# Kernel tuning notes

Measured on AMD Instinct MI355X. Metric: run time of the kernel, lower is better.

The kernel has to match this reference:

```python
import jax, jax.numpy as jnp
import numpy as np

B, T, K = 128, 512, 256  # batch, seq_len, num_tags


def setup_inputs() -> dict:
    key = jax.random.key(0)
    k1, k2, k3 = jax.random.split(key, 3)
    y_pred = jax.random.normal(k1, (B, T, K), dtype=jnp.float32)
    trans = jax.random.normal(k2, (K, K), dtype=jnp.float32)
    y_true = jax.random.randint(k3, (B, T), 0, K)
    return {"y_pred": y_pred, "trans": trans, "y_true": y_true}


def reference(y_pred, trans, y_true):
    # sparse_loss: one-hot the integer labels
    num_tags = trans.shape[0]
    y_oh = jax.nn.one_hot(y_true, num_tags, dtype=y_pred.dtype)  # [B,T,K]

    # dense_loss: mask frames where all logits <= -1e6
    mask = jnp.all(y_pred > -1e6, axis=2, keepdims=True).astype(y_pred.dtype)  # [B,T,1]
    y_oh = y_oh * mask
    yp = y_pred * mask

    # target_score: emission score + transition score along the gold path
    point_score = jnp.einsum('bti,bti->b', y_oh, yp)
    trans_score = jnp.einsum('bti,ij,btj->b', y_oh[:, :-1], trans, y_oh[:, 1:])
    target_score = point_score + trans_score  # [B]

    # log_norm_step: forward algorithm (log-semiring recurrence) via scan
    init = yp[:, 0]  # [B,K]

    def step(alpha, xm):
        x, m = xm  # x: [B,K] emissions at t, m: [B,1] mask at t
        # logsumexp over previous tag: alpha[b,i] + trans[i,j]
        new = jax.nn.logsumexp(alpha[:, :, None] + trans[None, :, :], axis=1) + x
        alpha = m * new + (1.0 - m) * alpha
        return alpha, None

    xs = (jnp.swapaxes(yp[:, 1:], 0, 1), jnp.swapaxes(mask[:, 1:], 0, 1))  # time-major
    last_alpha, _ = jax.lax.scan(step, init, xs)  # [B,K]
    log_norm = jax.nn.logsumexp(last_alpha, axis=1)  # [B]

    return log_norm - target_score  # per-example CRF negative log-likelihood [B]
```

## Files before the change

kernel.cpp:

```cpp
#include <hip/hip_runtime.h>
#include <stdint.h>

#define T_ 512
#define K_ 256
#define NB 16
#define WROW 264
#define L2E 1.4426950408889634f
#define LN2 0.6931471805599453f

typedef __attribute__((ext_vector_type(8))) short short8;
typedef __attribute__((ext_vector_type(4))) float f32x4;

__device__ __forceinline__ float fexp2(float x) {
#if __has_builtin(__builtin_amdgcn_exp2f)
  return __builtin_amdgcn_exp2f(x);
#else
  return exp2f(x);
#endif
}
__device__ __forceinline__ float flog2(float x) {
#if __has_builtin(__builtin_amdgcn_logf)
  return __builtin_amdgcn_logf(x);
#else
  return log2f(x);
#endif
}
__device__ __forceinline__ unsigned int umax_(unsigned int a, unsigned int b) {
  return a > b ? a : b;
}
__device__ __forceinline__ unsigned short f2bf(float f) {
  union { float f; uint32_t u; } v; v.f = f;
  uint32_t r = v.u + 0x7fffu + ((v.u >> 16) & 1u);
  return (unsigned short)(r >> 16);
}
__device__ __forceinline__ uint32_t cvt_pk_bf16(float a, float b) {
  uint32_t d;
  asm("v_cvt_pk_bf16_f32 %0, %1, %2" : "=v"(d) : "v"(a), "v"(b));
  return d;
}

#define BAR() do { \
  asm volatile("s_waitcnt lgkmcnt(0)" ::: "memory"); \
  __builtin_amdgcn_s_barrier(); \
  asm volatile("" ::: "memory"); \
} while (0)


__global__ void prep_E(const float* __restrict__ trans, unsigned short* __restrict__ Efrag) {
  int idx = blockIdx.x * 256 + threadIdx.x;
  int e = idx & 7;
  int ln = (idx >> 3) & 63;
  int kb = (idx >> 9) & 7;
  int mt = idx >> 12;
  int j = mt * 16 + (ln & 15);
  int k = kb * 32 + ((ln >> 4) << 3) + e;
  Efrag[idx] = f2bf(__expf(trans[k * K_ + j]));
}

__global__ void aux_mask(const float* __restrict__ yp, unsigned char* __restrict__ masks) {
  int item = blockIdx.x * 4 + (threadIdx.x >> 6);
  int lane = threadIdx.x & 63;
  const float4 v = *(const float4*)(yp + (size_t)item * K_ + lane * 4);
  float mn = fminf(fminf(v.x, v.y), fminf(v.z, v.w));
  unsigned long long bl = __ballot(mn > -1000000.0f);
  if (lane == 0) {
    int b = item >> 9, t = item & 511;
    masks[t * 128 + b] = (bl == ~0ull) ? 1 : 0;
  }
}

__global__ void aux_score(const float* __restrict__ yp, const float* __restrict__ trans,
                          const int* __restrict__ ytrue, const unsigned char* __restrict__ masks,
                          float* __restrict__ score) {
  int b = blockIdx.x;
  int lane = threadIdx.x;
  float s = 0.f;
  #pragma unroll
  for (int k = 0; k < 8; ++k) {
    int t = lane + 64 * k;
    int y = ytrue[b * T_ + t];
    int m = masks[t * 128 + b];
    float x = yp[((size_t)b * T_ + t) * K_ + y];
    if (m) s += x;
    if (t >= 1) {
      int ym = ytrue[b * T_ + t - 1];
      int mm = masks[(t - 1) * 128 + b];
      if (m && mm) s += trans[ym * K_ + y];
    }
  }
  #pragma unroll
  for (int off = 32; off; off >>= 1) s += __shfl_xor(s, off, 64);
  if (lane == 0) score[b] = s;
}


template<int TM4, bool RESC, bool MWR, bool MASKED>
__device__ __forceinline__ void crf_step(
    int t, int c, int g, int wv, const int* tb,
    const short8 (&Ef)[2][8],
    float (&a)[8], float (&exf)[8], int& acc, int& mkc,
    const float* xb, float4 (&XN)[2], float4 (&XI)[2],
    unsigned short (*Wl)[NB * WROW], const unsigned char* mkl, unsigned int* Mpart) {
  BAR();
  if (RESC) {
    unsigned int Mx = Mpart[c];
    #pragma unroll
    for (int w = 1; w < 8; ++w) Mx = umax_(Mx, Mpart[w * NB + c]);
    unsigned int e_ = Mx >> 23;
    float sf = __builtin_bit_cast(float, (254u - e_) << 23);
    if (!MASKED || mkc) acc += 127 - (int)e_;
    #pragma unroll
    for (int j = 0; j < 8; ++j) exf[j] *= sf;
  }
  f32x4 ac0 = {0.f, 0.f, 0.f, 0.f}, ac1 = {0.f, 0.f, 0.f, 0.f};
  {
    const unsigned short* rrow = &Wl[TM4 & 1][c * WROW];
    #pragma unroll
    for (int kb = 0; kb < 8; ++kb) {
      short8 bf = __builtin_bit_cast(short8, *(const uint4*)(&rrow[kb * 32 + g * 8]));
      ac0 = __builtin_amdgcn_mfma_f32_16x16x32_bf16(Ef[0][kb], bf, ac0, 0, 0, 0);
      ac1 = __builtin_amdgcn_mfma_f32_16x16x32_bf16(Ef[1][kb], bf, ac1, 0, 0, 0);
    }
  }
  if (MASKED) {
    #pragma unroll
    for (int i = 0; i < 4; ++i) { float an = ac0[i] * exf[i];     a[i]     = mkc ? an : a[i]; }
    #pragma unroll
    for (int i = 0; i < 4; ++i) { float an = ac1[i] * exf[4 + i]; a[4 + i] = mkc ? an : a[4 + i]; }
  } else {
    #pragma unroll
    for (int i = 0; i < 4; ++i) a[i]     = ac0[i] * exf[i];
    #pragma unroll
    for (int i = 0; i < 4; ++i) a[4 + i] = ac1[i] * exf[4 + i];
  }
  {
    unsigned short* wrow = &Wl[(TM4 + 1) & 1][c * WROW];
    #pragma unroll
    for (int m = 0; m < 2; ++m) {
      uint2 pp;
      pp.x = cvt_pk_bf16(a[4 * m + 0], a[4 * m + 1]);
      pp.y = cvt_pk_bf16(a[4 * m + 2], a[4 * m + 3]);
      *(uint2*)(&wrow[tb[m]]) = pp;
    }
  }
  if (MWR) {
    unsigned int pm = __builtin_bit_cast(uint32_t, a[0]);
    #pragma unroll
    for (int j = 1; j < 8; ++j) pm = umax_(pm, __builtin_bit_cast(uint32_t, a[j]));
    pm = umax_(pm, (unsigned int)__shfl_xor((int)pm, 16, 64));
    pm = umax_(pm, (unsigned int)__shfl_xor((int)pm, 32, 64));
    if (g == 0) Mpart[wv * NB + c] = pm;
  }
  #pragma unroll
  for (int m = 0; m < 2; ++m) {
    exf[4 * m + 0] = fexp2(XN[m].x * L2E);
    exf[4 * m + 1] = fexp2(XN[m].y * L2E);
    exf[4 * m + 2] = fexp2(XN[m].z * L2E);
    exf[4 * m + 3] = fexp2(XN[m].w * L2E);
  }
  if (MASKED) mkc = mkl[(t + 1 < T_ ? t + 1 : 0) * NB + c];
  {
    int tt = t + 4;
    tt = tt > (T_ - 1) ? (T_ - 1) : tt;
    #pragma unroll
    for (int m = 0; m < 2; ++m)
      XI[m] = *(const float4*)(xb + (size_t)tt * K_ + tb[m]);
  }
}

template<bool MASKED>
__device__ __forceinline__ void scan_run(
    int tid, int c, int g, int wv, const int* tb, int b0,
    const short8 (&Ef)[2][8], const float* xb,
    float4 (&xinit)[2], float4 (&X0q)[2], float4 (&X1q)[2],
    float4 (&X2q)[2], float4 (&X3q)[2],
    unsigned short (*Wl)[NB * WROW], const unsigned char* mkl,
    unsigned int* Mpart, float* Spart,
    const float* __restrict__ score, float* __restrict__ out) {
  float a[8], exf[8];
  int acc = 0;
  int mkc = 0;
  {
    int mk0 = MASKED ? mkl[c] : 1;
    #pragma unroll
    for (int m = 0; m < 2; ++m) {
      float e0 = fexp2(xinit[m].x * L2E);
      float e1 = fexp2(xinit[m].y * L2E);
      float e2 = fexp2(xinit[m].z * L2E);
      float e3 = fexp2(xinit[m].w * L2E);
      a[4 * m + 0] = (MASKED && !mk0) ? 1.0f : e0;
      a[4 * m + 1] = (MASKED && !mk0) ? 1.0f : e1;
      a[4 * m + 2] = (MASKED && !mk0) ? 1.0f : e2;
      a[4 * m + 3] = (MASKED && !mk0) ? 1.0f : e3;
    }
  }
  {
    unsigned short* wrow = &Wl[1][c * WROW];
    #pragma unroll
    for (int m = 0; m < 2; ++m) {
      uint2 pp;
      pp.x = cvt_pk_bf16(a[4 * m + 0], a[4 * m + 1]);
      pp.y = cvt_pk_bf16(a[4 * m + 2], a[4 * m + 3]);
      *(uint2*)(&wrow[tb[m]]) = pp;
    }
  }
  #pragma unroll
  for (int m = 0; m < 2; ++m) {
    exf[4 * m + 0] = fexp2(X1q[m].x * L2E);
    exf[4 * m + 1] = fexp2(X1q[m].y * L2E);
    exf[4 * m + 2] = fexp2(X1q[m].z * L2E);
    exf[4 * m + 3] = fexp2(X1q[m].w * L2E);
  }
  if (MASKED) mkc = mkl[NB + c];

  crf_step<1, false, false, MASKED>(1, c, g, wv, tb, Ef, a, exf, acc, mkc, xb, X2q, X1q, Wl, mkl, Mpart);
  crf_step<2, false, false, MASKED>(2, c, g, wv, tb, Ef, a, exf, acc, mkc, xb, X3q, X2q, Wl, mkl, Mpart);
  crf_step<3, false, true , MASKED>(3, c, g, wv, tb, Ef, a, exf, acc, mkc, xb, X0q, X3q, Wl, mkl, Mpart);

  #pragma unroll 1
  for (int t0 = 4; t0 < T_; t0 += 4) {
    crf_step<0, true , false, MASKED>(t0,     c, g, wv, tb, Ef, a, exf, acc, mkc, xb, X1q, X0q, Wl, mkl, Mpart);
    crf_step<1, false, false, MASKED>(t0 + 1, c, g, wv, tb, Ef, a, exf, acc, mkc, xb, X2q, X1q, Wl, mkl, Mpart);
    crf_step<2, false, false, MASKED>(t0 + 2, c, g, wv, tb, Ef, a, exf, acc, mkc, xb, X3q, X2q, Wl, mkl, Mpart);
    crf_step<3, false, true , MASKED>(t0 + 3, c, g, wv, tb, Ef, a, exf, acc, mkc, xb, X0q, X3q, Wl, mkl, Mpart);
  }

  __syncthreads();
  {
    float ssum = 0.f;
    #pragma unroll
    for (int j = 0; j < 8; ++j) ssum += a[j];
    ssum += __shfl_xor(ssum, 16, 64);
    ssum += __shfl_xor(ssum, 32, 64);
    if (g == 0) Spart[wv * NB + c] = ssum;
  }
  __syncthreads();
  if (tid < NB) {
    float S = 0.f;
    #pragma unroll
    for (int w = 0; w < 8; ++w) S += Spart[w * NB + tid];
    out[b0 + tid] = LN2 * (flog2(S) - (float)acc) - score[b0 + tid];
  }
}

__global__ __launch_bounds__(512, 1) void crf_scan(
    const float* __restrict__ yp, const unsigned short* __restrict__ Efrag,
    const unsigned char* __restrict__ masks, const float* __restrict__ score,
    float* __restrict__ out) {
  const int b0 = blockIdx.x * NB;
  const int tid = threadIdx.x;
  const int wv = tid >> 6, lane = tid & 63;
  const int c = lane & 15;
  const int g = lane >> 4;

  __shared__ unsigned short Wl[2][NB * WROW];
  __shared__ unsigned char mkl[T_ * NB];
  __shared__ unsigned int Mpart[8 * NB];
  __shared__ float Spart[8 * NB];
  __shared__ int sflag[8];

  short8 Ef[2][8];
  {
    const uint4* ep = (const uint4*)Efrag;
    #pragma unroll
    for (int m = 0; m < 2; ++m)
      #pragma unroll
      for (int kb = 0; kb < 8; ++kb)
        Ef[m][kb] = __builtin_bit_cast(short8, ep[((wv * 2 + m) * 8 + kb) * 64 + lane]);
  }

  uint4 md0;
  {
    uint4* dst = (uint4*)mkl;
    md0 = *(const uint4*)(masks + tid * 128 + b0);
    dst[tid] = md0;
  }

  const float* xb = yp + (size_t)(b0 + c) * T_ * K_;
  int tb[2];
  #pragma unroll
  for (int m = 0; m < 2; ++m) tb[m] = wv * 32 + m * 16 + g * 4;

  float4 xinit[2], X0q[2], X1q[2], X2q[2], X3q[2];
  #pragma unroll
  for (int m = 0; m < 2; ++m) xinit[m] = *(const float4*)(xb + tb[m]);
  #pragma unroll
  for (int m = 0; m < 2; ++m) X1q[m] = *(const float4*)(xb + 1 * K_ + tb[m]);
  #pragma unroll
  for (int m = 0; m < 2; ++m) X2q[m] = *(const float4*)(xb + 2 * K_ + tb[m]);
  #pragma unroll
  for (int m = 0; m < 2; ++m) X3q[m] = *(const float4*)(xb + 3 * K_ + tb[m]);
  #pragma unroll
  for (int m = 0; m < 2; ++m) X0q[m] = *(const float4*)(xb + 4 * K_ + tb[m]);

  {
    uint32_t w = md0.x & md0.y & md0.z & md0.w;
    unsigned long long bl = __ballot(w == 0x01010101u);
    if (lane == 0) sflag[wv] = (bl == ~0ull) ? 1 : 0;
  }
  __syncthreads();
  bool allm = true;
  #pragma unroll
  for (int w = 0; w < 8; ++w) allm = allm && sflag[w];

  if (allm) {
    scan_run<false>(tid, c, g, wv, tb, b0, Ef, xb, xinit, X0q, X1q, X2q, X3q,
                    Wl, mkl, Mpart, Spart, score, out);
  } else {
    scan_run<true>(tid, c, g, wv, tb, b0, Ef, xb, xinit, X0q, X1q, X2q, X3q,
                   Wl, mkl, Mpart, Spart, score, out);
  }
}

extern "C" void kernel_launch(void* const* d_in, const int* in_sizes, int n_in,
                              void* d_out, int out_size, void* d_ws, size_t ws_size,
                              hipStream_t stream) {
  const float* yp = (const float*)d_in[0];
  const float* trans = (const float*)d_in[1];
  const int* ytrue = (const int*)d_in[2];
  float* out = (float*)d_out;

  unsigned short* Efrag = (unsigned short*)d_ws;
  unsigned char* masks = (unsigned char*)d_ws + 131072;
  float* score = (float*)((char*)d_ws + 131072 + 65536);

  prep_E<<<dim3(256), dim3(256), 0, stream>>>(trans, Efrag);
  aux_mask<<<dim3(16384), dim3(256), 0, stream>>>(yp, masks);
  aux_score<<<dim3(128), dim3(64), 0, stream>>>(yp, trans, ytrue, masks, score);
  crf_scan<<<dim3(8), dim3(512), 0, stream>>>(yp, Efrag, masks, score, out);
}
```

Measured before the change: 302.0 us.

## Switch CRF scan recurrence to FP8 MFMA with per-step rescaling and precomputed exp emissions

Stores exp(trans) as e4m3 and the alpha vector as bf8 in LDS, so the recurrence uses the fp8×bf8 16x16x32 MFMA instead of bf16, halving the LDS and register traffic per step. Because bf8 has little dynamic range, rescaling by the running max now happens every step, using double-buffered partial maxima, instead of every fourth step. Emission exponentials are optionally precomputed as bf16 inside the mask kernel, which runs at full occupancy, when workspace allows, so the serial scan does less transcendental work and loads half the bytes. The cost is much lower numerical precision, which risks tolerance failures, plus an extra 32 MB workspace write and read.

```diff
diff --git a/kernel.cpp b/kernel.cpp
--- a/kernel.cpp
+++ b/kernel.cpp
@@ -4,11 +4,10 @@
 #define T_ 512
 #define K_ 256
 #define NB 16
-#define WROW 264
+#define WSTRIDE 272
 #define L2E 1.4426950408889634f
 #define LN2 0.6931471805599453f
 
-typedef __attribute__((ext_vector_type(8))) short short8;
 typedef __attribute__((ext_vector_type(4))) float f32x4;
 
 __device__ __forceinline__ float fexp2(float x) {
@@ -28,15 +27,48 @@
 __device__ __forceinline__ unsigned int umax_(unsigned int a, unsigned int b) {
   return a > b ? a : b;
 }
-__device__ __forceinline__ unsigned short f2bf(float f) {
-  union { float f; uint32_t u; } v; v.f = f;
-  uint32_t r = v.u + 0x7fffu + ((v.u >> 16) & 1u);
-  return (unsigned short)(r >> 16);
-}
+__device__ __forceinline__ float bits2f(uint32_t u) { return __builtin_bit_cast(float, u); }
+__device__ __forceinline__ uint32_t f2bits(float f) { return __builtin_bit_cast(uint32_t, f); }
+
 __device__ __forceinline__ uint32_t cvt_pk_bf16(float a, float b) {
   uint32_t d;
   asm("v_cvt_pk_bf16_f32 %0, %1, %2" : "=v"(d) : "v"(a), "v"(b));
   return d;
+}
+
+template<bool HI>
+__device__ __forceinline__ uint32_t pk_bf8(float a, float b, uint32_t old) {
+#if __has_builtin(__builtin_amdgcn_cvt_pk_bf8_f32)
+  return (uint32_t)__builtin_amdgcn_cvt_pk_bf8_f32(a, b, (int)old, HI);
+#else
+  unsigned short ha = __builtin_bit_cast(unsigned short, (_Float16)fminf(a, 57344.0f));
+  unsigned short hb = __builtin_bit_cast(unsigned short, (_Float16)fminf(b, 57344.0f));
+  uint32_t ra = (((uint32_t)ha + 0x7Fu + ((ha >> 8) & 1u)) >> 8) & 0xFFu;
+  uint32_t rb = (((uint32_t)hb + 0x7Fu + ((hb >> 8) & 1u)) >> 8) & 0xFFu;
+  uint32_t v = ra | (rb << 8);
+  return HI ? ((old & 0x0000FFFFu) | (v << 16)) : ((old & 0xFFFF0000u) | v);
+#endif
+}
+
+__device__ unsigned char to_e4m3(float f) {
+  if (!(f > 0.0f)) return 0;
+  if (f >= 448.0f) return 0x7E;
+  uint32_t u = f2bits(f);
+  int e = (int)((u >> 23) & 255) - 127;
+  uint32_t m = u & 0x7fffff;
+  if (e < -6) {
+    int s2 = 20 + (-6 - e);
+    if (s2 >= 24) return 0;
+    uint32_t full = 0x800000u | m;
+    uint32_t q = full >> s2, r = full & ((1u << s2) - 1);
+    uint32_t half = 1u << (s2 - 1);
+    q += (r > half || (r == half && (q & 1))) ? 1u : 0u;
+    return (unsigned char)q;
+  }
+  uint32_t q = m >> 20, r = m & 0xFFFFFu;
+  q += (r > 0x80000u || (r == 0x80000u && (q & 1))) ? 1u : 0u;
+  if (q == 8) { q = 0; e += 1; if (e > 8) return 0x7E; }
+  return (unsigned char)(((e + 7) << 3) | q);
 }
 
 #define BAR() do { \
@@ -46,7 +78,7 @@
 } while (0)
 
 
-__global__ void prep_E(const float* __restrict__ trans, unsigned short* __restrict__ Efrag) {
+__global__ void prep_E(const float* __restrict__ trans, unsigned char* __restrict__ Efrag) {
   int idx = blockIdx.x * 256 + threadIdx.x;
   int e = idx & 7;
   int ln = (idx >> 3) & 63;
@@ -54,10 +86,11 @@
   int mt = idx >> 12;
   int j = mt * 16 + (ln & 15);
   int k = kb * 32 + ((ln >> 4) << 3) + e;
-  Efrag[idx] = f2bf(__expf(trans[k * K_ + j]));
-}
-
-__global__ void aux_mask(const float* __restrict__ yp, unsigned char* __restrict__ masks) {
+  Efrag[idx] = to_e4m3(__expf(trans[k * K_ + j]));
+}
+
+__global__ void aux_mask_exf(const float* __restrict__ yp, unsigned char* __restrict__ masks,
+                             unsigned short* __restrict__ exf, int write_exf) {
   int item = blockIdx.x * 4 + (threadIdx.x >> 6);
   int lane = threadIdx.x & 63;
   const float4 v = *(const float4*)(yp + (size_t)item * K_ + lane * 4);
@@ -66,6 +99,12 @@
   if (lane == 0) {
     int b = item >> 9, t = item & 511;
     masks[t * 128 + b] = (bl == ~0ull) ? 1 : 0;
+  }
+  if (write_exf) {
+    uint2 p;
+    p.x = cvt_pk_bf16(fexp2(v.x * L2E), fexp2(v.y * L2E));
+    p.y = cvt_pk_bf16(fexp2(v.z * L2E), fexp2(v.w * L2E));
+    *(uint2*)(exf + (size_t)item * K_ + lane * 4) = p;
   }
 }
 
@@ -94,135 +133,168 @@
 }
 
 
-template<int TM4, bool RESC, bool MWR, bool MASKED>
+template<bool PRE> struct Slot;
+template<> struct Slot<true>  { uint2 u0, u1; };
+template<> struct Slot<false> { float4 f0, f1; };
+
+template<bool PRE>
+__device__ __forceinline__ void slot_load(Slot<PRE>& s, const void* base, int tt, int off0) {
+  if constexpr (PRE) {
+    const unsigned short* p = (const unsigned short*)base + (size_t)tt * K_ + off0;
+    s.u0 = *(const uint2*)(p);
+    s.u1 = *(const uint2*)(p + 16);
+  } else {
+    const float* p = (const float*)base + (size_t)tt * K_ + off0;
+    s.f0 = *(const float4*)(p);
+    s.f1 = *(const float4*)(p + 16);
+  }
+}
+
+template<bool PRE>
+__device__ __forceinline__ void slot_exf(const Slot<PRE>& s, float (&exf)[8]) {
+  if constexpr (PRE) {
+    exf[0] = bits2f(s.u0.x << 16); exf[1] = bits2f(s.u0.x & 0xffff0000u);
+    exf[2] = bits2f(s.u0.y << 16); exf[3] = bits2f(s.u0.y & 0xffff0000u);
+    exf[4] = bits2f(s.u1.x << 16); exf[5] = bits2f(s.u1.x & 0xffff0000u);
+    exf[6] = bits2f(s.u1.y << 16); exf[7] = bits2f(s.u1.y & 0xffff0000u);
+  } else {
+    exf[0] = fexp2(s.f0.x * L2E); exf[1] = fexp2(s.f0.y * L2E);
+    exf[2] = fexp2(s.f0.z * L2E); exf[3] = fexp2(s.f0.w * L2E);
+    exf[4] = fexp2(s.f1.x * L2E); exf[5] = fexp2(s.f1.y * L2E);
+    exf[6] = fexp2(s.f1.z * L2E); exf[7] = fexp2(s.f1.w * L2E);
+  }
+}
+
+__device__ __forceinline__ void pack_w(const float (&a)[8], unsigned char* wrow, int wv, int g) {
+  float s0 = fminf(a[0], 57344.f), s1 = fminf(a[1], 57344.f);
+  float s2 = fminf(a[2], 57344.f), s3 = fminf(a[3], 57344.f);
+  float s4 = fminf(a[4], 57344.f), s5 = fminf(a[5], 57344.f);
+  float s6 = fminf(a[6], 57344.f), s7 = fminf(a[7], 57344.f);
+  uint32_t u0 = pk_bf8<false>(s0, s1, 0u); u0 = pk_bf8<true>(s2, s3, u0);
+  uint32_t u1 = pk_bf8<false>(s4, s5, 0u); u1 = pk_bf8<true>(s6, s7, u1);
+  *(uint32_t*)(wrow + 32 * wv + 4 * g) = u0;
+  *(uint32_t*)(wrow + 32 * wv + 16 + 4 * g) = u1;
+}
+
+template<int TM4, bool MASKED, bool PRE>
 __device__ __forceinline__ void crf_step(
-    int t, int c, int g, int wv, const int* tb,
-    const short8 (&Ef)[2][8],
+    int t, int c, int g, int wv, int off0,
+    const uint2 (&Ef)[2][8],
     float (&a)[8], float (&exf)[8], int& acc, int& mkc,
-    const float* xb, float4 (&XN)[2], float4 (&XI)[2],
-    unsigned short (*Wl)[NB * WROW], const unsigned char* mkl, unsigned int* Mpart) {
+    const void* xbase, Slot<PRE>& XN, Slot<PRE>& XI,
+    unsigned char (*Wl)[NB * WSTRIDE], const unsigned char* mkl,
+    unsigned int (*Mpart)[NB][8]) {
   BAR();
-  if (RESC) {
-    unsigned int Mx = Mpart[c];
-    #pragma unroll
-    for (int w = 1; w < 8; ++w) Mx = umax_(Mx, Mpart[w * NB + c]);
-    unsigned int e_ = Mx >> 23;
-    float sf = __builtin_bit_cast(float, (254u - e_) << 23);
-    if (!MASKED || mkc) acc += 127 - (int)e_;
-    #pragma unroll
-    for (int j = 0; j < 8; ++j) exf[j] *= sf;
-  }
+  unsigned int Mx;
+  {
+    const uint4* mp = (const uint4*)&Mpart[(TM4 + 1) & 1][c][0];
+    uint4 m0 = mp[0], m1 = mp[1];
+    Mx = umax_(umax_(umax_(m0.x, m0.y), umax_(m0.z, m0.w)),
+               umax_(umax_(m1.x, m1.y), umax_(m1.z, m1.w)));
+  }
+  unsigned int e_ = Mx >> 23;
+  float sfp = bits2f((248u - e_) << 23);
+  int scur = 121 - (int)e_;
   f32x4 ac0 = {0.f, 0.f, 0.f, 0.f}, ac1 = {0.f, 0.f, 0.f, 0.f};
   {
-    const unsigned short* rrow = &Wl[TM4 & 1][c * WROW];
+    const unsigned char* rrow = &Wl[TM4 & 1][c * WSTRIDE];
     #pragma unroll
     for (int kb = 0; kb < 8; ++kb) {
-      short8 bf = __builtin_bit_cast(short8, *(const uint4*)(&rrow[kb * 32 + g * 8]));
-      ac0 = __builtin_amdgcn_mfma_f32_16x16x32_bf16(Ef[0][kb], bf, ac0, 0, 0, 0);
-      ac1 = __builtin_amdgcn_mfma_f32_16x16x32_bf16(Ef[1][kb], bf, ac1, 0, 0, 0);
+      long bf = *(const long*)(rrow + kb * 32 + g * 8);
+      ac0 = __builtin_amdgcn_mfma_f32_16x16x32_fp8_bf8(
+          __builtin_bit_cast(long, Ef[0][kb]), bf, ac0, 0, 0, 0);
+      ac1 = __builtin_amdgcn_mfma_f32_16x16x32_fp8_bf8(
+          __builtin_bit_cast(long, Ef[1][kb]), bf, ac1, 0, 0, 0);
     }
   }
   if (MASKED) {
     #pragma unroll
-    for (int i = 0; i < 4; ++i) { float an = ac0[i] * exf[i];     a[i]     = mkc ? an : a[i]; }
-    #pragma unroll
-    for (int i = 0; i < 4; ++i) { float an = ac1[i] * exf[4 + i]; a[4 + i] = mkc ? an : a[4 + i]; }
+    for (int i = 0; i < 4; ++i) { float an = ac0[i] * exf[i] * sfp;     a[i]     = mkc ? an : a[i]; }
+    #pragma unroll
+    for (int i = 0; i < 4; ++i) { float an = ac1[i] * exf[4 + i] * sfp; a[4 + i] = mkc ? an : a[4 + i]; }
+    if (mkc) acc += scur;
   } else {
     #pragma unroll
-    for (int i = 0; i < 4; ++i) a[i]     = ac0[i] * exf[i];
-    #pragma unroll
-    for (int i = 0; i < 4; ++i) a[4 + i] = ac1[i] * exf[4 + i];
-  }
-  {
-    unsigned short* wrow = &Wl[(TM4 + 1) & 1][c * WROW];
-    #pragma unroll
-    for (int m = 0; m < 2; ++m) {
-      uint2 pp;
-      pp.x = cvt_pk_bf16(a[4 * m + 0], a[4 * m + 1]);
-      pp.y = cvt_pk_bf16(a[4 * m + 2], a[4 * m + 3]);
-      *(uint2*)(&wrow[tb[m]]) = pp;
-    }
-  }
-  if (MWR) {
-    unsigned int pm = __builtin_bit_cast(uint32_t, a[0]);
-    #pragma unroll
-    for (int j = 1; j < 8; ++j) pm = umax_(pm, __builtin_bit_cast(uint32_t, a[j]));
+    for (int i = 0; i < 4; ++i) a[i]     = ac0[i] * exf[i] * sfp;
+    #pragma unroll
+    for (int i = 0; i < 4; ++i) a[4 + i] = ac1[i] * exf[4 + i] * sfp;
+    acc += scur;
+  }
+  pack_w(a, &Wl[(TM4 + 1) & 1][c * WSTRIDE], wv, g);
+  {
+    unsigned int pm = f2bits(a[0]);
+    #pragma unroll
+    for (int j = 1; j < 8; ++j) pm = umax_(pm, f2bits(a[j]));
     pm = umax_(pm, (unsigned int)__shfl_xor((int)pm, 16, 64));
     pm = umax_(pm, (unsigned int)__shfl_xor((int)pm, 32, 64));
-    if (g == 0) Mpart[wv * NB + c] = pm;
-  }
-  #pragma unroll
-  for (int m = 0; m < 2; ++m) {
-    exf[4 * m + 0] = fexp2(XN[m].x * L2E);
-    exf[4 * m + 1] = fexp2(XN[m].y * L2E);
-    exf[4 * m + 2] = fexp2(XN[m].z * L2E);
-    exf[4 * m + 3] = fexp2(XN[m].w * L2E);
-  }
+    if (g == 0) Mpart[TM4 & 1][c][wv] = pm;
+  }
+  slot_exf<PRE>(XN, exf);
   if (MASKED) mkc = mkl[(t + 1 < T_ ? t + 1 : 0) * NB + c];
   {
     int tt = t + 4;
     tt = tt > (T_ - 1) ? (T_ - 1) : tt;
-    #pragma unroll
-    for (int m = 0; m < 2; ++m)
-      XI[m] = *(const float4*)(xb + (size_t)tt * K_ + tb[m]);
-  }
-}
-
-template<bool MASKED>
+    slot_load<PRE>(XI, xbase, tt, off0);
+  }
+}
+
+template<bool MASKED, bool PRE>
 __device__ __forceinline__ void scan_run(
-    int tid, int c, int g, int wv, const int* tb, int b0,
-    const short8 (&Ef)[2][8], const float* xb,
-    float4 (&xinit)[2], float4 (&X0q)[2], float4 (&X1q)[2],
-    float4 (&X2q)[2], float4 (&X3q)[2],
-    unsigned short (*Wl)[NB * WROW], const unsigned char* mkl,
-    unsigned int* Mpart, float* Spart,
+    int tid, int c, int g, int wv, int off0, int b0,
+    const uint2 (&Ef)[2][8], const void* xbase,
+    Slot<PRE>& Sinit, Slot<PRE>& S0, Slot<PRE>& S1, Slot<PRE>& S2, Slot<PRE>& S3,
+    unsigned char (*Wl)[NB * WSTRIDE], const unsigned char* mkl,
+    unsigned int (*Mpart)[NB][8], float* Spart,
     const float* __restrict__ score, float* __restrict__ out) {
   float a[8], exf[8];
-  int acc = 0;
-  int mkc = 0;
-  {
+  int acc = 0, mkc = 0;
+  {
+    float e0[8];
+    slot_exf<PRE>(Sinit, e0);
     int mk0 = MASKED ? mkl[c] : 1;
     #pragma unroll
-    for (int m = 0; m < 2; ++m) {
-      float e0 = fexp2(xinit[m].x * L2E);
-      float e1 = fexp2(xinit[m].y * L2E);
-      float e2 = fexp2(xinit[m].z * L2E);
-      float e3 = fexp2(xinit[m].w * L2E);
-      a[4 * m + 0] = (MASKED && !mk0) ? 1.0f : e0;
-      a[4 * m + 1] = (MASKED && !mk0) ? 1.0f : e1;
-      a[4 * m + 2] = (MASKED && !mk0) ? 1.0f : e2;
-      a[4 * m + 3] = (MASKED && !mk0) ? 1.0f : e3;
-    }
-  }
-  {
-    unsigned short* wrow = &Wl[1][c * WROW];
-    #pragma unroll
-    for (int m = 0; m < 2; ++m) {
-      uint2 pp;
-      pp.x = cvt_pk_bf16(a[4 * m + 0], a[4 * m + 1]);
-      pp.y = cvt_pk_bf16(a[4 * m + 2], a[4 * m + 3]);
-      *(uint2*)(&wrow[tb[m]]) = pp;
-    }
-  }
+    for (int j = 0; j < 8; ++j) a[j] = (MASKED && !mk0) ? 1.0f : e0[j];
+  }
+  unsigned int pm0;
+  {
+    unsigned int pm = f2bits(a[0]);
+    #pragma unroll
+    for (int j = 1; j < 8; ++j) pm = umax_(pm, f2bits(a[j]));
+    pm = umax_(pm, (unsigned int)__shfl_xor((int)pm, 16, 64));
+    pm = umax_(pm, (unsigned int)__shfl_xor((int)pm, 32, 64));
+    pm0 = pm;
+    if (g == 0) Mpart[0][c][wv] = pm;
+  }
+  __syncthreads();
+  float sfp0;
+  {
+    unsigned int Mx;
+    const uint4* mp = (const uint4*)&Mpart[0][c][0];
+    uint4 m0 = mp[0], m1 = mp[1];
+    Mx = umax_(umax_(umax_(m0.x, m0.y), umax_(m0.z, m0.w)),
+               umax_(umax_(m1.x, m1.y), umax_(m1.z, m1.w)));
+    unsigned int e_ = Mx >> 23;
+    sfp0 = bits2f((248u - e_) << 23);
+    acc = 121 - (int)e_;
+  }
+  __syncthreads();
   #pragma unroll
-  for (int m = 0; m < 2; ++m) {
-    exf[4 * m + 0] = fexp2(X1q[m].x * L2E);
-    exf[4 * m + 1] = fexp2(X1q[m].y * L2E);
-    exf[4 * m + 2] = fexp2(X1q[m].z * L2E);
-    exf[4 * m + 3] = fexp2(X1q[m].w * L2E);
-  }
+  for (int j = 0; j < 8; ++j) a[j] *= sfp0;
+  if (g == 0) Mpart[0][c][wv] = f2bits(bits2f(pm0) * sfp0);
+  pack_w(a, &Wl[1][c * WSTRIDE], wv, g);
+  slot_exf<PRE>(S1, exf);
   if (MASKED) mkc = mkl[NB + c];
 
-  crf_step<1, false, false, MASKED>(1, c, g, wv, tb, Ef, a, exf, acc, mkc, xb, X2q, X1q, Wl, mkl, Mpart);
-  crf_step<2, false, false, MASKED>(2, c, g, wv, tb, Ef, a, exf, acc, mkc, xb, X3q, X2q, Wl, mkl, Mpart);
-  crf_step<3, false, true , MASKED>(3, c, g, wv, tb, Ef, a, exf, acc, mkc, xb, X0q, X3q, Wl, mkl, Mpart);
+  crf_step<1, MASKED, PRE>(1, c, g, wv, off0, Ef, a, exf, acc, mkc, xbase, S2, S1, Wl, mkl, Mpart);
+  crf_step<2, MASKED, PRE>(2, c, g, wv, off0, Ef, a, exf, acc, mkc, xbase, S3, S2, Wl, mkl, Mpart);
+  crf_step<3, MASKED, PRE>(3, c, g, wv, off0, Ef, a, exf, acc, mkc, xbase, S0, S3, Wl, mkl, Mpart);
 
   #pragma unroll 1
   for (int t0 = 4; t0 < T_; t0 += 4) {
-    crf_step<0, true , false, MASKED>(t0,     c, g, wv, tb, Ef, a, exf, acc, mkc, xb, X1q, X0q, Wl, mkl, Mpart);
-    crf_step<1, false, false, MASKED>(t0 + 1, c, g, wv, tb, Ef, a, exf, acc, mkc, xb, X2q, X1q, Wl, mkl, Mpart);
-    crf_step<2, false, false, MASKED>(t0 + 2, c, g, wv, tb, Ef, a, exf, acc, mkc, xb, X3q, X2q, Wl, mkl, Mpart);
-    crf_step<3, false, true , MASKED>(t0 + 3, c, g, wv, tb, Ef, a, exf, acc, mkc, xb, X0q, X3q, Wl, mkl, Mpart);
+    crf_step<0, MASKED, PRE>(t0,     c, g, wv, off0, Ef, a, exf, acc, mkc, xbase, S1, S0, Wl, mkl, Mpart);
+    crf_step<1, MASKED, PRE>(t0 + 1, c, g, wv, off0, Ef, a, exf, acc, mkc, xbase, S2, S1, Wl, mkl, Mpart);
+    crf_step<2, MASKED, PRE>(t0 + 2, c, g, wv, off0, Ef, a, exf, acc, mkc, xbase, S3, S2, Wl, mkl, Mpart);
+    crf_step<3, MASKED, PRE>(t0 + 3, c, g, wv, off0, Ef, a, exf, acc, mkc, xbase, S0, S3, Wl, mkl, Mpart);
   }
 
   __syncthreads();
@@ -243,30 +315,32 @@
   }
 }
 
+template<bool PRE>
 __global__ __launch_bounds__(512, 1) void crf_scan(
-    const float* __restrict__ yp, const unsigned short* __restrict__ Efrag,
-    const unsigned char* __restrict__ masks, const float* __restrict__ score,
-    float* __restrict__ out) {
+    const float* __restrict__ yp, const unsigned char* __restrict__ Efrag,
+    const unsigned char* __restrict__ masks, const unsigned short* __restrict__ exfp,
+    const float* __restrict__ score, float* __restrict__ out) {
   const int b0 = blockIdx.x * NB;
   const int tid = threadIdx.x;
   const int wv = tid >> 6, lane = tid & 63;
   const int c = lane & 15;
   const int g = lane >> 4;
-
-  __shared__ unsigned short Wl[2][NB * WROW];
+  const int off0 = 32 * wv + 4 * g;
+
+  __shared__ unsigned char Wl[2][NB * WSTRIDE];
   __shared__ unsigned char mkl[T_ * NB];
-  __shared__ unsigned int Mpart[8 * NB];
+  __shared__ unsigned int Mpart[2][NB][8];
   __shared__ float Spart[8 * NB];
   __shared__ int sflag[8];
 
-  short8 Ef[2][8];
-  {
-    const uint4* ep = (const uint4*)Efrag;
+  uint2 Ef[2][8];
+  {
+    const uint2* ep = (const uint2*)Efrag;
     #pragma unroll
     for (int m = 0; m < 2; ++m)
       #pragma unroll
       for (int kb = 0; kb < 8; ++kb)
-        Ef[m][kb] = __builtin_bit_cast(short8, ep[((wv * 2 + m) * 8 + kb) * 64 + lane]);
+        Ef[m][kb] = ep[((wv * 2 + m) * 8 + kb) * 64 + lane];
   }
 
   uint4 md0;
@@ -276,22 +350,16 @@
     dst[tid] = md0;
   }
 
-  const float* xb = yp + (size_t)(b0 + c) * T_ * K_;
-  int tb[2];
-  #pragma unroll
-  for (int m = 0; m < 2; ++m) tb[m] = wv * 32 + m * 16 + g * 4;
-
-  float4 xinit[2], X0q[2], X1q[2], X2q[2], X3q[2];
-  #pragma unroll
-  for (int m = 0; m < 2; ++m) xinit[m] = *(const float4*)(xb + tb[m]);
-  #pragma unroll
-  for (int m = 0; m < 2; ++m) X1q[m] = *(const float4*)(xb + 1 * K_ + tb[m]);
-  #pragma unroll
-  for (int m = 0; m < 2; ++m) X2q[m] = *(const float4*)(xb + 2 * K_ + tb[m]);
-  #pragma unroll
-  for (int m = 0; m < 2; ++m) X3q[m] = *(const float4*)(xb + 3 * K_ + tb[m]);
-  #pragma unroll
-  for (int m = 0; m < 2; ++m) X0q[m] = *(const float4*)(xb + 4 * K_ + tb[m]);
+  const void* xbase;
+  if constexpr (PRE) xbase = (const void*)(exfp + (size_t)(b0 + c) * T_ * K_);
+  else               xbase = (const void*)(yp + (size_t)(b0 + c) * T_ * K_);
+
+  Slot<PRE> Sinit, S0, S1, S2, S3;
+  slot_load<PRE>(Sinit, xbase, 0, off0);
+  slot_load<PRE>(S1, xbase, 1, off0);
+  slot_load<PRE>(S2, xbase, 2, off0);
+  slot_load<PRE>(S3, xbase, 3, off0);
+  slot_load<PRE>(S0, xbase, 4, off0);
 
   {
     uint32_t w = md0.x & md0.y & md0.z & md0.w;
@@ -304,11 +372,11 @@
   for (int w = 0; w < 8; ++w) allm = allm && sflag[w];
 
   if (allm) {
-    scan_run<false>(tid, c, g, wv, tb, b0, Ef, xb, xinit, X0q, X1q, X2q, X3q,
-                    Wl, mkl, Mpart, Spart, score, out);
+    scan_run<false, PRE>(tid, c, g, wv, off0, b0, Ef, xbase, Sinit, S0, S1, S2, S3,
+                         Wl, mkl, Mpart, Spart, score, out);
   } else {
-    scan_run<true>(tid, c, g, wv, tb, b0, Ef, xb, xinit, X0q, X1q, X2q, X3q,
-                   Wl, mkl, Mpart, Spart, score, out);
+    scan_run<true, PRE>(tid, c, g, wv, off0, b0, Ef, xbase, Sinit, S0, S1, S2, S3,
+                        Wl, mkl, Mpart, Spart, score, out);
   }
 }
 
@@ -320,12 +388,20 @@
   const int* ytrue = (const int*)d_in[2];
   float* out = (float*)d_out;
 
-  unsigned short* Efrag = (unsigned short*)d_ws;
-  unsigned char* masks = (unsigned char*)d_ws + 131072;
-  float* score = (float*)((char*)d_ws + 131072 + 65536);
+  unsigned char* Efrag = (unsigned char*)d_ws;
+  unsigned char* masks = (unsigned char*)d_ws + 65536;
+  float* score = (float*)((char*)d_ws + 131072);
+  unsigned short* exf = (unsigned short*)((char*)d_ws + 131584);
+
+  const size_t exf_bytes = (size_t)128 * T_ * K_ * sizeof(unsigned short);
+  const bool pre = ws_size >= 131584 + exf_bytes;
 
   prep_E<<<dim3(256), dim3(256), 0, stream>>>(trans, Efrag);
-  aux_mask<<<dim3(16384), dim3(256), 0, stream>>>(yp, masks);
+  aux_mask_exf<<<dim3(16384), dim3(256), 0, stream>>>(yp, masks, exf, pre ? 1 : 0);
   aux_score<<<dim3(128), dim3(64), 0, stream>>>(yp, trans, ytrue, masks, score);
-  crf_scan<<<dim3(8), dim3(512), 0, stream>>>(yp, Efrag, masks, score, out);
-}
+  if (pre) {
+    crf_scan<true><<<dim3(8), dim3(512), 0, stream>>>(yp, Efrag, masks, exf, score, out);
+  } else {
+    crf_scan<false><<<dim3(8), dim3(512), 0, stream>>>(yp, Efrag, masks, exf, score, out);
+  }
+}
```

Result: slower. 321.0 us (+6.3%).

## Interleave two independent 16-sequence scans per block to hide step latency

Applied to the files above, without the earlier changes.

Each block now processes 32 sequences as two independent groups (A and B), interleaving their recurrence steps between shared barriers so the MFMA, exp and LDS latency of one group can overlap the other. The grid shrinks from 8 to 4 blocks, the mask staging uses a 32-wide stride, and barriers move out of crf_step so one barrier covers both groups. The trade-off is fewer active CUs and more registers and LDS per block, in exchange for better latency hiding within each block.

```diff
diff --git a/kernel.cpp b/kernel.cpp
--- a/kernel.cpp
+++ b/kernel.cpp
@@ -4,6 +4,7 @@
 #define T_ 512
 #define K_ 256
 #define NB 16
+#define MKS 32
 #define WROW 264
 #define L2E 1.4426950408889634f
 #define LN2 0.6931471805599453f
@@ -28,6 +29,9 @@
 __device__ __forceinline__ unsigned int umax_(unsigned int a, unsigned int b) {
   return a > b ? a : b;
 }
+__device__ __forceinline__ float bits2f(uint32_t u) { return __builtin_bit_cast(float, u); }
+__device__ __forceinline__ uint32_t f2bits(float f) { return __builtin_bit_cast(uint32_t, f); }
+
 __device__ __forceinline__ unsigned short f2bf(float f) {
   union { float f; uint32_t u; } v; v.f = f;
   uint32_t r = v.u + 0x7fffu + ((v.u >> 16) & 1u);
@@ -101,13 +105,12 @@
     float (&a)[8], float (&exf)[8], int& acc, int& mkc,
     const float* xb, float4 (&XN)[2], float4 (&XI)[2],
     unsigned short (*Wl)[NB * WROW], const unsigned char* mkl, unsigned int* Mpart) {
-  BAR();
   if (RESC) {
     unsigned int Mx = Mpart[c];
     #pragma unroll
     for (int w = 1; w < 8; ++w) Mx = umax_(Mx, Mpart[w * NB + c]);
     unsigned int e_ = Mx >> 23;
-    float sf = __builtin_bit_cast(float, (254u - e_) << 23);
+    float sf = bits2f((254u - e_) << 23);
     if (!MASKED || mkc) acc += 127 - (int)e_;
     #pragma unroll
     for (int j = 0; j < 8; ++j) exf[j] *= sf;
@@ -144,9 +147,9 @@
     }
   }
   if (MWR) {
-    unsigned int pm = __builtin_bit_cast(uint32_t, a[0]);
-    #pragma unroll
-    for (int j = 1; j < 8; ++j) pm = umax_(pm, __builtin_bit_cast(uint32_t, a[j]));
+    unsigned int pm = f2bits(a[0]);
+    #pragma unroll
+    for (int j = 1; j < 8; ++j) pm = umax_(pm, f2bits(a[j]));
     pm = umax_(pm, (unsigned int)__shfl_xor((int)pm, 16, 64));
     pm = umax_(pm, (unsigned int)__shfl_xor((int)pm, 32, 64));
     if (g == 0) Mpart[wv * NB + c] = pm;
@@ -158,7 +161,7 @@
     exf[4 * m + 2] = fexp2(XN[m].z * L2E);
     exf[4 * m + 3] = fexp2(XN[m].w * L2E);
   }
-  if (MASKED) mkc = mkl[(t + 1 < T_ ? t + 1 : 0) * NB + c];
+  if (MASKED) mkc = mkl[(t + 1 < T_ ? t + 1 : 0) * MKS + c];
   {
     int tt = t + 4;
     tt = tt > (T_ - 1) ? (T_ - 1) : tt;
@@ -167,79 +170,120 @@
       XI[m] = *(const float4*)(xb + (size_t)tt * K_ + tb[m]);
   }
 }
+
 
 template<bool MASKED>
 __device__ __forceinline__ void scan_run(
     int tid, int c, int g, int wv, const int* tb, int b0,
-    const short8 (&Ef)[2][8], const float* xb,
-    float4 (&xinit)[2], float4 (&X0q)[2], float4 (&X1q)[2],
-    float4 (&X2q)[2], float4 (&X3q)[2],
-    unsigned short (*Wl)[NB * WROW], const unsigned char* mkl,
-    unsigned int* Mpart, float* Spart,
+    const short8 (&Ef)[2][8],
+    const float* xbA, const float* xbB,
+    unsigned short (*WlA)[NB * WROW], unsigned short (*WlB)[NB * WROW],
+    const unsigned char* mklA, const unsigned char* mklB,
+    unsigned int* MpA, unsigned int* MpB, float* SpA, float* SpB,
     const float* __restrict__ score, float* __restrict__ out) {
-  float a[8], exf[8];
-  int acc = 0;
-  int mkc = 0;
-  {
-    int mk0 = MASKED ? mkl[c] : 1;
+  float aA[8], exfA[8], aB[8], exfB[8];
+  int accA = 0, mkcA = 0, accB = 0, mkcB = 0;
+  float4 A0[2], A1[2], A2[2], A3[2];
+  float4 B0[2], B1[2], B2[2], B3[2];
+
+  {
+    float4 xiA[2], xiB[2];
     #pragma unroll
     for (int m = 0; m < 2; ++m) {
-      float e0 = fexp2(xinit[m].x * L2E);
-      float e1 = fexp2(xinit[m].y * L2E);
-      float e2 = fexp2(xinit[m].z * L2E);
-      float e3 = fexp2(xinit[m].w * L2E);
-      a[4 * m + 0] = (MASKED && !mk0) ? 1.0f : e0;
-      a[4 * m + 1] = (MASKED && !mk0) ? 1.0f : e1;
-      a[4 * m + 2] = (MASKED && !mk0) ? 1.0f : e2;
-      a[4 * m + 3] = (MASKED && !mk0) ? 1.0f : e3;
-    }
-  }
-  {
-    unsigned short* wrow = &Wl[1][c * WROW];
+      xiA[m] = *(const float4*)(xbA + tb[m]);
+      xiB[m] = *(const float4*)(xbB + tb[m]);
+      A1[m] = *(const float4*)(xbA + 1 * K_ + tb[m]);
+      B1[m] = *(const float4*)(xbB + 1 * K_ + tb[m]);
+      A2[m] = *(const float4*)(xbA + 2 * K_ + tb[m]);
+      B2[m] = *(const float4*)(xbB + 2 * K_ + tb[m]);
+      A3[m] = *(const float4*)(xbA + 3 * K_ + tb[m]);
+      B3[m] = *(const float4*)(xbB + 3 * K_ + tb[m]);
+      A0[m] = *(const float4*)(xbA + 4 * K_ + tb[m]);
+      B0[m] = *(const float4*)(xbB + 4 * K_ + tb[m]);
+    }
+    int mkA0 = MASKED ? mklA[c] : 1;
+    int mkB0 = MASKED ? mklB[c] : 1;
     #pragma unroll
     for (int m = 0; m < 2; ++m) {
-      uint2 pp;
-      pp.x = cvt_pk_bf16(a[4 * m + 0], a[4 * m + 1]);
-      pp.y = cvt_pk_bf16(a[4 * m + 2], a[4 * m + 3]);
-      *(uint2*)(&wrow[tb[m]]) = pp;
+      aA[4 * m + 0] = (MASKED && !mkA0) ? 1.0f : fexp2(xiA[m].x * L2E);
+      aA[4 * m + 1] = (MASKED && !mkA0) ? 1.0f : fexp2(xiA[m].y * L2E);
+      aA[4 * m + 2] = (MASKED && !mkA0) ? 1.0f : fexp2(xiA[m].z * L2E);
+      aA[4 * m + 3] = (MASKED && !mkA0) ? 1.0f : fexp2(xiA[m].w * L2E);
+      aB[4 * m + 0] = (MASKED && !mkB0) ? 1.0f : fexp2(xiB[m].x * L2E);
+      aB[4 * m + 1] = (MASKED && !mkB0) ? 1.0f : fexp2(xiB[m].y * L2E);
+      aB[4 * m + 2] = (MASKED && !mkB0) ? 1.0f : fexp2(xiB[m].z * L2E);
+      aB[4 * m + 3] = (MASKED && !mkB0) ? 1.0f : fexp2(xiB[m].w * L2E);
+    }
+  }
+  {
+    unsigned short* wrA = &WlA[1][c * WROW];
+    unsigned short* wrB = &WlB[1][c * WROW];
+    #pragma unroll
+    for (int m = 0; m < 2; ++m) {
+      uint2 pa, pb;
+      pa.x = cvt_pk_bf16(aA[4 * m + 0], aA[4 * m + 1]);
+      pa.y = cvt_pk_bf16(aA[4 * m + 2], aA[4 * m + 3]);
+      pb.x = cvt_pk_bf16(aB[4 * m + 0], aB[4 * m + 1]);
+      pb.y = cvt_pk_bf16(aB[4 * m + 2], aB[4 * m + 3]);
+      *(uint2*)(&wrA[tb[m]]) = pa;
+      *(uint2*)(&wrB[tb[m]]) = pb;
     }
   }
   #pragma unroll
   for (int m = 0; m < 2; ++m) {
-    exf[4 * m + 0] = fexp2(X1q[m].x * L2E);
-    exf[4 * m + 1] = fexp2(X1q[m].y * L2E);
-    exf[4 * m + 2] = fexp2(X1q[m].z * L2E);
-    exf[4 * m + 3] = fexp2(X1q[m].w * L2E);
-  }
-  if (MASKED) mkc = mkl[NB + c];
-
-  crf_step<1, false, false, MASKED>(1, c, g, wv, tb, Ef, a, exf, acc, mkc, xb, X2q, X1q, Wl, mkl, Mpart);
-  crf_step<2, false, false, MASKED>(2, c, g, wv, tb, Ef, a, exf, acc, mkc, xb, X3q, X2q, Wl, mkl, Mpart);
-  crf_step<3, false, true , MASKED>(3, c, g, wv, tb, Ef, a, exf, acc, mkc, xb, X0q, X3q, Wl, mkl, Mpart);
+    exfA[4 * m + 0] = fexp2(A1[m].x * L2E);
+    exfA[4 * m + 1] = fexp2(A1[m].y * L2E);
+    exfA[4 * m + 2] = fexp2(A1[m].z * L2E);
+    exfA[4 * m + 3] = fexp2(A1[m].w * L2E);
+    exfB[4 * m + 0] = fexp2(B1[m].x * L2E);
+    exfB[4 * m + 1] = fexp2(B1[m].y * L2E);
+    exfB[4 * m + 2] = fexp2(B1[m].z * L2E);
+    exfB[4 * m + 3] = fexp2(B1[m].w * L2E);
+  }
+  if (MASKED) { mkcA = mklA[MKS + c]; mkcB = mklB[MKS + c]; }
+
+  BAR();
+  crf_step<1, false, false, MASKED>(1, c, g, wv, tb, Ef, aA, exfA, accA, mkcA, xbA, A2, A1, WlA, mklA, MpA);
+  crf_step<1, false, false, MASKED>(1, c, g, wv, tb, Ef, aB, exfB, accB, mkcB, xbB, B2, B1, WlB, mklB, MpB);
+  BAR();
+  crf_step<2, false, false, MASKED>(2, c, g, wv, tb, Ef, aA, exfA, accA, mkcA, xbA, A3, A2, WlA, mklA, MpA);
+  crf_step<2, false, false, MASKED>(2, c, g, wv, tb, Ef, aB, exfB, accB, mkcB, xbB, B3, B2, WlB, mklB, MpB);
+  BAR();
+  crf_step<3, false, true , MASKED>(3, c, g, wv, tb, Ef, aA, exfA, accA, mkcA, xbA, A0, A3, WlA, mklA, MpA);
+  crf_step<3, false, true , MASKED>(3, c, g, wv, tb, Ef, aB, exfB, accB, mkcB, xbB, B0, B3, WlB, mklB, MpB);
 
   #pragma unroll 1
   for (int t0 = 4; t0 < T_; t0 += 4) {
-    crf_step<0, true , false, MASKED>(t0,     c, g, wv, tb, Ef, a, exf, acc, mkc, xb, X1q, X0q, Wl, mkl, Mpart);
-    crf_step<1, false, false, MASKED>(t0 + 1, c, g, wv, tb, Ef, a, exf, acc, mkc, xb, X2q, X1q, Wl, mkl, Mpart);
-    crf_step<2, false, false, MASKED>(t0 + 2, c, g, wv, tb, Ef, a, exf, acc, mkc, xb, X3q, X2q, Wl, mkl, Mpart);
-    crf_step<3, false, true , MASKED>(t0 + 3, c, g, wv, tb, Ef, a, exf, acc, mkc, xb, X0q, X3q, Wl, mkl, Mpart);
+    BAR();
+    crf_step<0, true , false, MASKED>(t0,     c, g, wv, tb, Ef, aA, exfA, accA, mkcA, xbA, A1, A0, WlA, mklA, MpA);
+    crf_step<0, true , false, MASKED>(t0,     c, g, wv, tb, Ef, aB, exfB, accB, mkcB, xbB, B1, B0, WlB, mklB, MpB);
+    BAR();
+    crf_step<1, false, false, MASKED>(t0 + 1, c, g, wv, tb, Ef, aA, exfA, accA, mkcA, xbA, A2, A1, WlA, mklA, MpA);
+    crf_step<1, false, false, MASKED>(t0 + 1, c, g, wv, tb, Ef, aB, exfB, accB, mkcB, xbB, B2, B1, WlB, mklB, MpB);
+    BAR();
+    crf_step<2, false, false, MASKED>(t0 + 2, c, g, wv, tb, Ef, aA, exfA, accA, mkcA, xbA, A3, A2, WlA, mklA, MpA);
+    crf_step<2, false, false, MASKED>(t0 + 2, c, g, wv, tb, Ef, aB, exfB, accB, mkcB, xbB, B3, B2, WlB, mklB, MpB);
+    BAR();
+    crf_step<3, false, true , MASKED>(t0 + 3, c, g, wv, tb, Ef, aA, exfA, accA, mkcA, xbA, A0, A3, WlA, mklA, MpA);
+    crf_step<3, false, true , MASKED>(t0 + 3, c, g, wv, tb, Ef, aB, exfB, accB, mkcB, xbB, B0, B3, WlB, mklB, MpB);
   }
 
   __syncthreads();
   {
-    float ssum = 0.f;
-    #pragma unroll
-    for (int j = 0; j < 8; ++j) ssum += a[j];
-    ssum += __shfl_xor(ssum, 16, 64);
-    ssum += __shfl_xor(ssum, 32, 64);
-    if (g == 0) Spart[wv * NB + c] = ssum;
+    float sA = 0.f, sB = 0.f;
+    #pragma unroll
+    for (int j = 0; j < 8; ++j) { sA += aA[j]; sB += aB[j]; }
+    sA += __shfl_xor(sA, 16, 64); sA += __shfl_xor(sA, 32, 64);
+    sB += __shfl_xor(sB, 16, 64); sB += __shfl_xor(sB, 32, 64);
+    if (g == 0) { SpA[wv * NB + c] = sA; SpB[wv * NB + c] = sB; }
   }
   __syncthreads();
   if (tid < NB) {
-    float S = 0.f;
-    #pragma unroll
-    for (int w = 0; w < 8; ++w) S += Spart[w * NB + tid];
-    out[b0 + tid] = LN2 * (flog2(S) - (float)acc) - score[b0 + tid];
+    float SA = 0.f, SB = 0.f;
+    #pragma unroll
+    for (int w = 0; w < 8; ++w) { SA += SpA[w * NB + tid]; SB += SpB[w * NB + tid]; }
+    out[b0 + tid] = LN2 * (flog2(SA) - (float)accA) - score[b0 + tid];
+    out[b0 + NB + tid] = LN2 * (flog2(SB) - (float)accB) - score[b0 + NB + tid];
   }
 }
 
@@ -247,16 +291,19 @@
     const float* __restrict__ yp, const unsigned short* __restrict__ Efrag,
     const unsigned char* __restrict__ masks, const float* __restrict__ score,
     float* __restrict__ out) {
-  const int b0 = blockIdx.x * NB;
+  const int b0 = blockIdx.x * 32;
   const int tid = threadIdx.x;
   const int wv = tid >> 6, lane = tid & 63;
   const int c = lane & 15;
   const int g = lane >> 4;
 
-  __shared__ unsigned short Wl[2][NB * WROW];
-  __shared__ unsigned char mkl[T_ * NB];
-  __shared__ unsigned int Mpart[8 * NB];
-  __shared__ float Spart[8 * NB];
+  __shared__ unsigned short WlA[2][NB * WROW];
+  __shared__ unsigned short WlB[2][NB * WROW];
+  __shared__ unsigned char mkl[T_ * MKS];
+  __shared__ unsigned int MpA[8 * NB];
+  __shared__ unsigned int MpB[8 * NB];
+  __shared__ float SpA[8 * NB];
+  __shared__ float SpB[8 * NB];
   __shared__ int sflag[8];
 
   short8 Ef[2][8];
@@ -269,32 +316,22 @@
         Ef[m][kb] = __builtin_bit_cast(short8, ep[((wv * 2 + m) * 8 + kb) * 64 + lane]);
   }
 
-  uint4 md0;
-  {
-    uint4* dst = (uint4*)mkl;
+  uint4 md0, md1;
+  {
     md0 = *(const uint4*)(masks + tid * 128 + b0);
-    dst[tid] = md0;
-  }
-
-  const float* xb = yp + (size_t)(b0 + c) * T_ * K_;
+    md1 = *(const uint4*)(masks + tid * 128 + b0 + 16);
+    *(uint4*)(&mkl[tid * MKS]) = md0;
+    *(uint4*)(&mkl[tid * MKS + 16]) = md1;
+  }
+
+  const float* xbA = yp + (size_t)(b0 + c) * T_ * K_;
+  const float* xbB = yp + (size_t)(b0 + 16 + c) * T_ * K_;
   int tb[2];
   #pragma unroll
   for (int m = 0; m < 2; ++m) tb[m] = wv * 32 + m * 16 + g * 4;
 
-  float4 xinit[2], X0q[2], X1q[2], X2q[2], X3q[2];
-  #pragma unroll
-  for (int m = 0; m < 2; ++m) xinit[m] = *(const float4*)(xb + tb[m]);
-  #pragma unroll
-  for (int m = 0; m < 2; ++m) X1q[m] = *(const float4*)(xb + 1 * K_ + tb[m]);
-  #pragma unroll
-  for (int m = 0; m < 2; ++m) X2q[m] = *(const float4*)(xb + 2 * K_ + tb[m]);
-  #pragma unroll
-  for (int m = 0; m < 2; ++m) X3q[m] = *(const float4*)(xb + 3 * K_ + tb[m]);
-  #pragma unroll
-  for (int m = 0; m < 2; ++m) X0q[m] = *(const float4*)(xb + 4 * K_ + tb[m]);
-
-  {
-    uint32_t w = md0.x & md0.y & md0.z & md0.w;
+  {
+    uint32_t w = md0.x & md0.y & md0.z & md0.w & md1.x & md1.y & md1.z & md1.w;
     unsigned long long bl = __ballot(w == 0x01010101u);
     if (lane == 0) sflag[wv] = (bl == ~0ull) ? 1 : 0;
   }
@@ -304,11 +341,11 @@
   for (int w = 0; w < 8; ++w) allm = allm && sflag[w];
 
   if (allm) {
-    scan_run<false>(tid, c, g, wv, tb, b0, Ef, xb, xinit, X0q, X1q, X2q, X3q,
-                    Wl, mkl, Mpart, Spart, score, out);
+    scan_run<false>(tid, c, g, wv, tb, b0, Ef, xbA, xbB, WlA, WlB,
+                    mkl, mkl + 16, MpA, MpB, SpA, SpB, score, out);
   } else {
-    scan_run<true>(tid, c, g, wv, tb, b0, Ef, xb, xinit, X0q, X1q, X2q, X3q,
-                   Wl, mkl, Mpart, Spart, score, out);
+    scan_run<true>(tid, c, g, wv, tb, b0, Ef, xbA, xbB, WlA, WlB,
+                   mkl, mkl + 16, MpA, MpB, SpA, SpB, score, out);
   }
 }
 
@@ -327,5 +364,5 @@
   prep_E<<<dim3(256), dim3(256), 0, stream>>>(trans, Efrag);
   aux_mask<<<dim3(16384), dim3(256), 0, stream>>>(yp, masks);
   aux_score<<<dim3(128), dim3(64), 0, stream>>>(yp, trans, ytrue, masks, score);
-  crf_scan<<<dim3(8), dim3(512), 0, stream>>>(yp, Efrag, masks, score, out);
-}
+  crf_scan<<<dim3(4), dim3(512), 0, stream>>>(yp, Efrag, masks, score, out);
+}
```

Measured after the change: 480.3 us. +59.0%, slower.
